# Optimization experiments

Hardware: AMD Instinct MI355X
Metric: run time of the kernel (lower is better)

Reference implementation:

```python
import jax, jax.numpy as jnp
import numpy as np

B, N, K = 4, 1500, 30
NODE_F, EDGE_F, H = 1024, 128, 128
L, NUM_RBF, NUM_POS, NHEADS = 4, 16, 16, 4
DH = H // NHEADS
LN_EPS = 1e-6


def setup_inputs() -> dict:
    key = jax.random.key(0)
    ks = jax.random.split(key, 16)
    g = lambda k, shp: jax.random.normal(k, shp, jnp.float32) / np.sqrt(shp[-2] if len(shp) > 1 else 1.0)
    return {
        'X': jax.random.normal(ks[0], (B, N, 3), jnp.float32) * 10.0,
        'V': jax.random.normal(ks[1], (B, N, NODE_F), jnp.float32),
        'mask': jnp.ones((B, N), jnp.float32),
        'W_v': g(ks[2], (NODE_F, H)), 'b_v': jnp.zeros((H,), jnp.float32),
        'W_e': g(ks[3], (EDGE_F, H)), 'b_e': jnp.zeros((H,), jnp.float32),
        'W_edge': g(ks[4], (NUM_POS + NUM_RBF, EDGE_F)),
        'ln_e_g': jnp.ones((EDGE_F,), jnp.float32), 'ln_e_b': jnp.zeros((EDGE_F,), jnp.float32),
        'Wq': g(ks[5], (L, H, H)), 'Wk': g(ks[6], (L, 2 * H, H)),
        'Wv_a': g(ks[7], (L, 2 * H, H)), 'Wo': g(ks[8], (L, H, H)),
        'ln1_g': jnp.ones((L, H), jnp.float32), 'ln1_b': jnp.zeros((L, H), jnp.float32),
        'ln2_g': jnp.ones((L, H), jnp.float32), 'ln2_b': jnp.zeros((L, H), jnp.float32),
        'W_ff1': g(ks[9], (L, H, 4 * H)), 'b_ff1': jnp.zeros((L, 4 * H), jnp.float32),
        'W_ff2': g(ks[10], (L, 4 * H, H)), 'b_ff2': jnp.zeros((L, H), jnp.float32),
        'W_out': g(ks[11], (H, 1)), 'b_out': jnp.zeros((1,), jnp.float32),
    }


def _layer_norm(x, gamma, beta):
    mu = jnp.mean(x, -1, keepdims=True)
    var = jnp.var(x, -1, keepdims=True)
    return gamma * (x - mu) / jnp.sqrt(var + LN_EPS) + beta


def _gather_nodes(nodes, idx):
    # nodes [B,N,C], idx [B,N,K] -> [B,N,K,C]
    return jax.vmap(lambda n, i: n[i])(nodes, idx)


def reference(X, V, mask, W_v, b_v, W_e, b_e, W_edge, ln_e_g, ln_e_b, Wq, Wk, Wv_a, Wo,
              ln1_g, ln1_b, ln2_g, ln2_b, W_ff1, b_ff1, W_ff2, b_ff2, W_out, b_out):
    # ---- EdgeFeatures: masked pairwise distances + kNN topk ----
    mask2 = mask[:, :, None] * mask[:, None, :]            # [B,N,N]
    dX = X[:, :, None, :] - X[:, None, :, :]               # [B,N,N,3]
    D = mask2 * jnp.sqrt(jnp.sum(dX * dX, -1) + 1e-6)
    D_adj = D + (1.0 - mask2) * jnp.max(D, -1, keepdims=True)
    negD, E_idx = jax.lax.top_k(-D_adj, K)                 # k smallest distances
    D_nb = -negD                                           # [B,N,K]
    # RBF of neighbor distances
    mu = jnp.linspace(0.0, 20.0, NUM_RBF)
    sigma = 20.0 / NUM_RBF
    rbf = jnp.exp(-(((D_nb[..., None] - mu) / sigma) ** 2))  # [B,N,K,NUM_RBF]
    # sinusoidal relative positional encodings of neighbor offsets
    ii = jnp.arange(N, dtype=jnp.float32)[None, :, None]
    d_rel = (E_idx.astype(jnp.float32) - ii)[..., None]
    freq = jnp.exp(jnp.arange(0, NUM_POS, 2, dtype=jnp.float32) * (-np.log(10000.0) / NUM_POS))
    ang = d_rel * freq
    pos = jnp.concatenate([jnp.cos(ang), jnp.sin(ang)], -1)  # [B,N,K,NUM_POS]
    E = jnp.concatenate([pos, rbf], -1) @ W_edge
    E = _layer_norm(E, ln_e_g, ln_e_b)                     # [B,N,K,EDGE_F]
    # ---- node / edge embeddings ----
    h_V = V @ W_v + b_v                                    # [B,N,H]
    h_E = E @ W_e + b_e                                    # [B,N,K,H]
    mask_attend = mask[:, :, None] * _gather_nodes(mask[..., None], E_idx)[..., 0]  # [B,N,K]
    neg_inf = jnp.float32(np.finfo(np.float32).min)
    # ---- encoder layers ----
    for l in range(L):
        h_EV = jnp.concatenate([h_E, _gather_nodes(h_V, E_idx)], -1)  # [B,N,K,2H]
        Q = (h_V @ Wq[l]).reshape(B, N, NHEADS, DH)
        Kh = (h_EV @ Wk[l]).reshape(B, N, K, NHEADS, DH)
        Vh = (h_EV @ Wv_a[l]).reshape(B, N, K, NHEADS, DH)
        logits = jnp.einsum('bnhd,bnkhd->bnhk', Q, Kh) / np.sqrt(DH)
        m = mask_attend[:, :, None, :]                     # [B,N,1,K]
        attend = jax.nn.softmax(jnp.where(m > 0, logits, neg_inf), -1) * m
        upd = jnp.einsum('bnhk,bnkhd->bnhd', attend, Vh).reshape(B, N, H) @ Wo[l]
        h_V = _layer_norm(h_V + upd, ln1_g[l], ln1_b[l])
        dh = jax.nn.relu(h_V @ W_ff1[l] + b_ff1[l]) @ W_ff2[l] + b_ff2[l]
        h_V = _layer_norm(h_V + dh, ln2_g[l], ln2_b[l])
        h_V = mask[..., None] * h_V
    return (h_V @ W_out + b_out)[..., 0]                   # [B,N] logits
```

## Files before the change

### kernel.cpp

```cpp
#include <hip/hip_runtime.h>
#include <hip/hip_bf16.h>
#include <math.h>

#define NB 4
#define NN 1500
#define KNB 30
#define H 128
#define NHEADS 4
#define FFH 512
#define NODE_FEAT 1024
#define NROWS (NB*NN)
#define LN_EPS 1e-6f

#define P_F32_STRIDE 384
#define P_BF16_STRIDE 768

#define WNT_STRIDE 67584

typedef __attribute__((ext_vector_type(8))) short s8v;
typedef __attribute__((ext_vector_type(4))) float f4v;

__device__ __forceinline__ float bf_lo(unsigned u){ union{unsigned i; float f;} v; v.i = u<<16; return v.f; }
__device__ __forceinline__ float bf_hi(unsigned u){ union{unsigned i; float f;} v; v.i = u & 0xffff0000u; return v.f; }

__device__ __forceinline__ void find_bucket30(
    const unsigned* hist, int base0, int t, int lane, int wave,
    int* wsum, int* res)
{
    int h[16], s = 0;
    const uint4* hp = (const uint4*)&hist[(t & 127) * 16];
    int sh = (t >> 7) << 4;
    uint4 w[4] = {hp[0], hp[1], hp[2], hp[3]};
#pragma unroll
    for (int i = 0; i < 4; i++) {
        h[i*4+0] = (w[i].x >> sh) & 0xffff;
        h[i*4+1] = (w[i].y >> sh) & 0xffff;
        h[i*4+2] = (w[i].z >> sh) & 0xffff;
        h[i*4+3] = (w[i].w >> sh) & 0xffff;
        s += h[i*4+0] + h[i*4+1] + h[i*4+2] + h[i*4+3];
    }
    int inc = s;
#pragma unroll
    for (int off = 1; off < 64; off <<= 1) {
        int o = __shfl_up(inc, off, 64);
        if (lane >= off) inc += o;
    }
    if (lane == 63) wsum[wave] = inc;
    __syncthreads();
    int base = base0 + inc - s;
    for (int w2 = 0; w2 < wave; w2++) base += wsum[w2];
    if (base < KNB && base + s >= KNB) {
        int running = base;
#pragma unroll
        for (int i = 0; i < 16; i++) {
            if (running < KNB && running + h[i] >= KNB) { res[0] = (t<<4)|i; res[1] = running; break; }
            running += h[i];
        }
    }
    __syncthreads();
}

__global__ __launch_bounds__(256) void topk_kernel(
    const float* __restrict__ X, const float* __restrict__ mask,
    int* __restrict__ E_idx, float* __restrict__ D_nb)
{
    int row = blockIdx.x;
    int b = row / NN;
    int t = threadIdx.x;
    int wave = t >> 6, lane = t & 63;
    __shared__ float d_adj[NN];
    __shared__ unsigned hist[2048];
    __shared__ float redw[4];
    __shared__ int   wsum[4];
    __shared__ int   res[2];
    __shared__ int   cand[64];
    __shared__ int   ncand;

    float xi0 = X[row*3+0], xi1 = X[row*3+1], xi2 = X[row*3+2];
    float mi = mask[row];

    float dr[6], m2r[6];
    float lmax = -1e30f;
#pragma unroll
    for (int q = 0; q < 6; q++) {
        int j = t + q*256;
        float d = 0.f, m2 = 0.f;
        if (j < NN) {
            float dx = xi0 - X[(b*NN+j)*3+0];
            float dy = xi1 - X[(b*NN+j)*3+1];
            float dz = xi2 - X[(b*NN+j)*3+2];
            d  = sqrtf(dx*dx + dy*dy + dz*dz + 1e-6f);
            m2 = mi * mask[b*NN+j];
            lmax = fmaxf(lmax, m2*d);
        }
        dr[q] = d; m2r[q] = m2;
    }
    for (int q = t; q < 2048; q += 256) hist[q] = 0;
#pragma unroll
    for (int off = 32; off > 0; off >>= 1)
        lmax = fmaxf(lmax, __shfl_xor(lmax, off, 64));
    if (lane == 0) redw[wave] = lmax;
    if (t == 0) ncand = 0;
    __syncthreads();
    float rowmax = fmaxf(fmaxf(redw[0], redw[1]), fmaxf(redw[2], redw[3]));

    unsigned kreg[6];
#pragma unroll
    for (int q = 0; q < 6; q++) {
        int j = t + q*256;
        if (j < NN) {
            float dv = m2r[q]*dr[q] + (1.0f - m2r[q])*rowmax;
            d_adj[j] = dv;
            unsigned key = __float_as_uint(dv);
            kreg[q] = key;
            unsigned bkt = key >> 20;
            atomicAdd(&hist[bkt & 2047], 1u << ((bkt >> 11) << 4));
        } else kreg[q] = 0xFFFFFFFFu;
    }
    __syncthreads();

    find_bucket30(hist, 0, t, lane, wave, wsum, res);
    int B1 = res[0], nb1 = res[1];

    for (int q = t; q < 2048; q += 256) hist[q] = 0;
    __syncthreads();
#pragma unroll
    for (int q = 0; q < 6; q++) {
        if ((kreg[q] >> 20) == (unsigned)B1) {
            unsigned bkt = (kreg[q] >> 8) & 0xFFF;
            atomicAdd(&hist[bkt & 2047], 1u << ((bkt >> 11) << 4));
        }
    }
    __syncthreads();

    find_bucket30(hist, nb1, t, lane, wave, wsum, res);
    unsigned Bfull = ((unsigned)B1 << 12) | (unsigned)res[0];

#pragma unroll
    for (int q = 0; q < 6; q++) {
        if ((kreg[q] >> 8) <= Bfull) {
            int slot = atomicAdd(&ncand, 1);
            if (slot < 64) cand[slot] = t + q*256;
        }
    }
    __syncthreads();

    if (wave == 0) {
        int nc = min(ncand, 64);
        if (lane < nc) {
            int j = cand[lane];
            float v = d_adj[j];
            int rank = 0;
            for (int m = 0; m < nc; m++) {
                int jm = cand[m];
                float vm = d_adj[jm];
                rank += (vm < v || (vm == v && jm < j)) ? 1 : 0;
            }
            if (rank < KNB) {
                E_idx[row*KNB + rank] = j;
                D_nb[row*KNB + rank]  = v;
            }
        }
    }
}

__global__ __launch_bounds__(256) void wprep_edge_kernel(
    const float* __restrict__ W_edge, __hip_bfloat16* __restrict__ W_edge_t)
{
    int tid = blockIdx.x*256 + threadIdx.x;
    int n = tid >> 5, k = tid & 31;
    W_edge_t[tid] = __float2bfloat16(W_edge[k*H + n]);
}

__global__ __launch_bounds__(256) void edge_kernel(
    const int* __restrict__ E_idx, const float* __restrict__ D_nb,
    const __hip_bfloat16* __restrict__ W_edge_t, const float* __restrict__ ln_g,
    const float* __restrict__ ln_b, __hip_bfloat16* __restrict__ E_ln,
    float* __restrict__ EMS)
{
    int g0 = blockIdx.x * 2;
    int t = threadIdx.x;
    int wave = t >> 6, lane = t & 63, lm = lane & 15, lq = lane >> 4;
    __shared__ __hip_bfloat16 Es[64*136];

    int row = wave*16 + lm;
    int rr = row < 60 ? row : 59;
    int node = g0 + (rr >= KNB ? 1 : 0);
    int e = node*KNB + (rr >= KNB ? rr - KNB : rr);
    float drel = (float)(E_idx[e] - (node % NN));
    float dnb  = D_nb[e];

    const float FR[8] = {1.f, 0.31622776601683794f, 0.1f, 0.031622776601683794f,
                         0.01f, 0.0031622776601683794f, 0.001f, 0.00031622776601683794f};
    union { s8v v; __hip_bfloat16 h[8]; } af;
    if (lq == 0) {
#pragma unroll
        for (int j = 0; j < 8; j++) af.h[j] = __float2bfloat16(cosf(drel*FR[j]));
    } else if (lq == 1) {
#pragma unroll
        for (int j = 0; j < 8; j++) af.h[j] = __float2bfloat16(sinf(drel*FR[j]));
    } else {
        int f0 = (lq-2)*8;
#pragma unroll
        for (int j = 0; j < 8; j++) {
            float mu = (20.0f/15.0f) * (float)(f0+j);
            float z = (dnb - mu) * 0.8f;
            af.h[j] = __float2bfloat16(expf(-z*z));
        }
    }

    f4v acc[8];
#pragma unroll
    for (int nt = 0; nt < 8; nt++) {
        s8v bf = *(const s8v*)&W_edge_t[(nt*16+lm)*32 + lq*8];
        f4v z = {0.f,0.f,0.f,0.f};
        acc[nt] = __builtin_amdgcn_mfma_f32_16x16x32_bf16(af.v, bf, z, 0,0,0);
    }

    float gv[8], bv[8];
#pragma unroll
    for (int nt = 0; nt < 8; nt++) { gv[nt] = ln_g[nt*16+lm]; bv[nt] = ln_b[nt*16+lm]; }
#pragma unroll
    for (int r = 0; r < 4; r++) {
        float sm = 0.f, sq = 0.f;
#pragma unroll
        for (int nt = 0; nt < 8; nt++) { float x = acc[nt][r]; sm += x; sq += x*x; }
#pragma unroll
        for (int m = 1; m < 16; m <<= 1) {
            sm += __shfl_xor(sm, m, 64);
            sq += __shfl_xor(sq, m, 64);
        }
        float mu = sm * (1.0f/H);
        float rs = rsqrtf(sq*(1.0f/H) - mu*mu + LN_EPS);
        int erow = wave*16 + lq*4 + r;
        if (lm == 0 && erow < 60) {
            EMS[(g0*KNB + erow)*2]     = rs;
            EMS[(g0*KNB + erow)*2 + 1] = mu*rs;
        }
#pragma unroll
        for (int nt = 0; nt < 8; nt++)
            Es[erow*136 + nt*16 + lm] =
                __float2bfloat16(gv[nt]*(acc[nt][r]-mu)*rs + bv[nt]);
    }
    __syncthreads();

    __hip_bfloat16* dst = E_ln + (size_t)g0*KNB*H;
    for (int q = t; q < 960; q += 256) {
        int r = q >> 4, c8 = (q & 15) * 8;
        *(s8v*)&dst[r*H + c8] = *(const s8v*)&Es[r*136 + c8];
    }
}

__global__ __launch_bounds__(256) void wprep_v_kernel(
    const float* __restrict__ W_v, __hip_bfloat16* __restrict__ Wv_t)
{
    int tid = blockIdx.x*256 + threadIdx.x;
    int n = tid & 127, k = tid >> 7;
    Wv_t[(size_t)n*NODE_FEAT + k] = __float2bfloat16(W_v[k*H + n]);
}

__global__ __launch_bounds__(128) void wprep_kv_kernel(
    const float* __restrict__ W_e, const float* __restrict__ b_e,
    const float* __restrict__ Wk, const float* __restrict__ Wv,
    float* __restrict__ Wkv_f, float* __restrict__ bias_kv)
{
    int l = blockIdx.x >> 8;
    int n = blockIdx.x & 255;
    int t = threadIdx.x;
    int col = n & 127;
    const float* W = (n < 128) ? (Wk + l*2*H*H) : (Wv + l*2*H*H);
    __shared__ float wcol[128];
    wcol[t] = W[t*H + col];
    __syncthreads();
    float a = 0.f;
    for (int c = 0; c < H; c += 4) {
        float4 we = *(const float4*)&W_e[t*H + c];
        a += we.x*wcol[c] + we.y*wcol[c+1] + we.z*wcol[c+2] + we.w*wcol[c+3];
    }
    Wkv_f[(size_t)(l*256 + n)*H + t] = a;
    if (t == 0) {
        float bsum = 0.f;
        for (int c = 0; c < H; c++) bsum += b_e[c]*wcol[c];
        bias_kv[l*256 + n] = bsum;
    }
}

__global__ __launch_bounds__(128) void wprep_m_kernel(
    const float* __restrict__ Wkv_f, const float* __restrict__ W_edge,
    const float* __restrict__ ln_e_g,
    float* __restrict__ M_buf, float* __restrict__ vg_buf)
{
    int l = blockIdx.x >> 7;
    int n = blockIdx.x & 127;
    int t = threadIdx.x;
    __shared__ float wg_s[128];
    wg_s[t] = Wkv_f[(size_t)(l*256 + n)*H + t] * ln_e_g[t];
    __syncthreads();
    if (t < 32) {
        float a = 0.f;
        for (int e = 0; e < 128; e++) a += wg_s[e] * W_edge[t*H + e];
        M_buf[((size_t)(l*128 + n))*32 + t] = a;
    } else if (t == 32) {
        float a = 0.f;
        for (int e = 0; e < 128; e++) a += wg_s[e];
        vg_buf[l*128 + n] = a;
    }
}

__global__ __launch_bounds__(128) void wprep_q2_kernel(
    const float* __restrict__ Wq, const float* __restrict__ M_buf,
    const float* __restrict__ vg_buf, __hip_bfloat16* __restrict__ Wn_t)
{
    int l = blockIdx.x >> 7;
    int c = blockIdx.x & 127;
    int t = threadIdx.x;
    int h = t >> 5, f = t & 31;
    __shared__ float wq_s[128];
    wq_s[t] = Wq[(size_t)l*16384 + c*128 + t];
    __syncthreads();
    float a = 0.f;
#pragma unroll
    for (int d = 0; d < 32; d++)
        a += wq_s[h*32 + d] * M_buf[((size_t)(l*128 + h*32 + d))*32 + f];
    Wn_t[(size_t)l*WNT_STRIDE + (128 + t)*H + c] = __float2bfloat16(a);
    if (t < 4) {
        float b = 0.f;
        for (int d = 0; d < 32; d++)
            b += wq_s[t*32 + d] * vg_buf[l*128 + t*32 + d];
        Wn_t[(size_t)l*WNT_STRIDE + (256 + t)*H + c] = __float2bfloat16(b);
    }
    if (t < 12) Wn_t[(size_t)l*WNT_STRIDE + (260 + t)*H + c] = __float2bfloat16(0.f);
}

__global__ __launch_bounds__(128) void wprep_op_kernel(
    const float* __restrict__ Wo, const float* __restrict__ Wkv_f,
    __hip_bfloat16* __restrict__ WoU_t)
{
    int l = blockIdx.x / 640;
    int kk = blockIdx.x - l*640;
    int n = threadIdx.x;
    __shared__ float wev[32];
    if (kk < 512) {
        int h = kk >> 7;
        int e = kk & 127;
        if (n < 32) wev[n] = Wkv_f[(size_t)(l*256 + 128 + h*32 + n)*H + e];
    }
    __syncthreads();
    float v;
    if (kk < 512) {
        int h = kk >> 7;
        float a = 0.f;
#pragma unroll
        for (int d = 0; d < 32; d++)
            a += wev[d]*Wo[(size_t)l*16384 + (h*32+d)*128 + n];
        v = a;
    } else {
        v = Wo[(size_t)l*16384 + (kk-512)*128 + n];
    }
    WoU_t[((size_t)l*128 + n)*640 + kk] = __float2bfloat16(v);
}

__global__ __launch_bounds__(256) void wprep_post_kernel(
    const float* __restrict__ Wf1, const float* __restrict__ Wf2,
    const float* __restrict__ Wq, const float* __restrict__ Wk,
    const float* __restrict__ Wv,
    __hip_bfloat16* __restrict__ Wf1_t, __hip_bfloat16* __restrict__ Wf2_t,
    __hip_bfloat16* __restrict__ Wn_t)
{
    int id = blockIdx.x*256 + threadIdx.x;
    int l = id / 180224;
    int r = id - l*180224;
    float v; __hip_bfloat16* dst;
    if (r < 65536) {
        int n = r >> 7, k = r & 127;
        v = Wf1[(size_t)l*65536 + k*512 + n];
        dst = Wf1_t + (size_t)l*65536 + r;
    } else if (r < 131072) {
        int rr = r - 65536;
        int n = rr >> 9, k = rr & 511;
        v = Wf2[(size_t)l*65536 + k*128 + n];
        dst = Wf2_t + (size_t)l*65536 + rr;
    } else if (r < 147456) {
        int rr = r - 131072;
        int n = rr >> 7, k = rr & 127;
        v = Wq[(size_t)l*16384 + k*128 + n];
        dst = Wn_t + (size_t)l*WNT_STRIDE + rr;
    } else {
        int rr = r - 147456;
        int n = rr >> 7, k = rr & 127;
        v = (n < 128) ? Wk[(size_t)l*32768 + (128+k)*128 + n]
                      : Wv[(size_t)l*32768 + (128+k)*128 + (n-128)];
        dst = Wn_t + (size_t)l*WNT_STRIDE + 272*H + rr;
    }
    *dst = __float2bfloat16(v);
}

__global__ __launch_bounds__(512) void hv_init_kernel(
    const float* __restrict__ V, const __hip_bfloat16* __restrict__ Wv_t,
    const float* __restrict__ b_v, float* __restrict__ hv,
    const __hip_bfloat16* __restrict__ Wn_t, float* __restrict__ P,
    __hip_bfloat16* __restrict__ PKV, float* __restrict__ qg_buf)
{
    int row0 = blockIdx.x * 32;
    int t = threadIdx.x;
    int wave = t >> 6, lane = t & 63, lm = lane & 15, lq = lane >> 4;
    __shared__ __hip_bfloat16 Vs[32*1032];
    __shared__ __hip_bfloat16 zs[32*136];

    for (int q = t; q < 8192; q += 512) {
        int r = q >> 8, c4 = (q & 255) * 4;
        int gr = row0 + r; if (gr > NROWS-1) gr = NROWS-1;
        float4 v4 = *(const float4*)&V[(size_t)gr*NODE_FEAT + c4];
        union { ushort u[4]; uint2 w; } pk;
        pk.u[0] = __bfloat16_as_ushort(__float2bfloat16(v4.x));
        pk.u[1] = __bfloat16_as_ushort(__float2bfloat16(v4.y));
        pk.u[2] = __bfloat16_as_ushort(__float2bfloat16(v4.z));
        pk.u[3] = __bfloat16_as_ushort(__float2bfloat16(v4.w));
        *(uint2*)&Vs[r*1032 + c4] = pk.w;
    }
    __syncthreads();

    {
        int cc = wave*16 + lm;
        float b = b_v[cc];
        f4v a0 = {0.f,0.f,0.f,0.f}, a1 = a0;
        for (int ks = 0; ks < 32; ks++) {
            s8v wf = *(const s8v*)&Wv_t[(size_t)(wave*16+lm)*NODE_FEAT + ks*32 + lq*8];
            s8v f0 = *(const s8v*)&Vs[lm*1032 + ks*32 + lq*8];
            s8v f1 = *(const s8v*)&Vs[(16+lm)*1032 + ks*32 + lq*8];
            a0 = __builtin_amdgcn_mfma_f32_16x16x32_bf16(f0, wf, a0, 0,0,0);
            a1 = __builtin_amdgcn_mfma_f32_16x16x32_bf16(f1, wf, a1, 0,0,0);
        }
#pragma unroll
        for (int r = 0; r < 4; r++) {
            int rr0 = lq*4 + r, rr1 = 16 + lq*4 + r;
            int g0 = row0 + rr0, g1 = row0 + rr1;
            float v0 = a0[r] + b, v1 = a1[r] + b;
            if (g0 < NROWS) hv[(size_t)g0*H + cc] = v0;
            if (g1 < NROWS) hv[(size_t)g1*H + cc] = v1;
            zs[rr0*136+cc] = __float2bfloat16(v0);
            zs[rr1*136+cc] = __float2bfloat16(v1);
        }
    }
    __syncthreads();

    __hip_bfloat16* Pb = (__hip_bfloat16*)P;
    for (int ntl = 0; ntl < 5; ntl++) {
        int nt = wave*5 + ntl;
        if (nt >= 33) break;
        int cc = nt*16 + lm;
        f4v a0 = {0.f,0.f,0.f,0.f}, a1 = a0;
#pragma unroll
        for (int ks = 0; ks < 4; ks++) {
            s8v wf = *(const s8v*)&Wn_t[(size_t)(nt*16+lm)*H + ks*32 + lq*8];
            s8v f0 = *(const s8v*)&zs[lm*136 + ks*32 + lq*8];
            s8v f1 = *(const s8v*)&zs[(16+lm)*136 + ks*32 + lq*8];
            a0 = __builtin_amdgcn_mfma_f32_16x16x32_bf16(f0, wf, a0, 0,0,0);
            a1 = __builtin_amdgcn_mfma_f32_16x16x32_bf16(f1, wf, a1, 0,0,0);
        }
#pragma unroll
        for (int mt = 0; mt < 2; mt++) {
            f4v* ap = mt ? &a1 : &a0;
#pragma unroll
            for (int r = 0; r < 4; r++) {
                int rr = row0 + mt*16 + lq*4 + r;
                if (rr < NROWS) {
                    float av = (*ap)[r];
                    if (cc < 128)
                        P[(size_t)rr*P_F32_STRIDE + cc] = av;
                    else if (cc < 256)
                        Pb[(size_t)rr*P_BF16_STRIDE + 640 + (cc-128)] = __float2bfloat16(av);
                    else if (cc < 272) {
                        if (cc < 260) qg_buf[rr*4 + (cc-256)] = av;
                    } else
                        PKV[(size_t)rr*256 + (cc-272)] = __float2bfloat16(av);
                }
            }
        }
    }
}

__global__ __launch_bounds__(256) void attn_kernel(
    const __hip_bfloat16* __restrict__ E_ln, const float* __restrict__ biasv,
    float* __restrict__ P, const __hip_bfloat16* __restrict__ PKV,
    const int* __restrict__ E_idx, const float* __restrict__ D_nb,
    const float* __restrict__ EMS, const float* __restrict__ qg_buf,
    const float* __restrict__ mask)
{
    int g0 = blockIdx.x * 2;
    int t = threadIdx.x;
    int wave = t >> 6, lane = t & 63, lm = lane & 15, lq = lane >> 4;
    __shared__ __hip_bfloat16 Es[60*136];
    __shared__ __hip_bfloat16 Ps[60*40];
    __shared__ __hip_bfloat16 Qps[2*136];
    __shared__ float Qs[2*128];
    __shared__ float att_s[2*128];
    __shared__ float ssum[8];
    __shared__ float mv_s[60];
    __shared__ float rs_s[60], murs_s[60];
    __shared__ float qgs[8];
    __shared__ int   nbr[60];

    const __hip_bfloat16* hebase = E_ln + (size_t)g0*KNB*H;
    for (int q = t; q < 960; q += 256) {
        int r = q >> 4, c8 = (q & 15) * 8;
        *(s8v*)&Es[r*136 + c8] = *(const s8v*)&hebase[r*H + c8];
    }
    const __hip_bfloat16* Pb = (const __hip_bfloat16*)P;
    if (t < 32) {
        int node = t >> 4, c8 = (t & 15)*8;
        *(s8v*)&Qps[node*136 + c8] = *(const s8v*)&Pb[(size_t)(g0+node)*P_BF16_STRIDE + 640 + c8];
    }
    {
        int node = t >> 7, c = t & 127;
        Qs[t] = P[(size_t)(g0+node)*P_F32_STRIDE + c];
    }
    if (t < 60) {
        int gn = g0 + t/30;
        int b = gn / NN;
        int idx = E_idx[gn*KNB + (t%30)];
        nbr[t]  = b*NN + idx;
        mv_s[t] = mask[gn] * mask[b*NN + idx];
        float2 em = ((const float2*)EMS)[g0*KNB + t];
        rs_s[t] = em.x; murs_s[t] = em.y;
    }
    if (t < 8) qgs[t] = qg_buf[(g0 + (t>>2))*4 + (t&3)];
    if (t < 240) {
        int r = t >> 2, seg = t & 3;
        int gn = g0 + r/30;
        int e = gn*KNB + (r%30);
        float drel = (float)(E_idx[e] - (gn % NN));
        float dnb  = D_nb[e];
        const float FR[8] = {1.f, 0.31622776601683794f, 0.1f, 0.031622776601683794f,
                             0.01f, 0.0031622776601683794f, 0.001f, 0.00031622776601683794f};
        union { s8v v; __hip_bfloat16 h[8]; } pf;
        if (seg == 0) {
#pragma unroll
            for (int j = 0; j < 8; j++) pf.h[j] = __float2bfloat16(__cosf(drel*FR[j]));
        } else if (seg == 1) {
#pragma unroll
            for (int j = 0; j < 8; j++) pf.h[j] = __float2bfloat16(__sinf(drel*FR[j]));
        } else {
            int f0 = (seg-2)*8;
#pragma unroll
            for (int j = 0; j < 8; j++) {
                float mu = (20.0f/15.0f) * (float)(f0+j);
                float z = (dnb - mu) * 0.8f;
                pf.h[j] = __float2bfloat16(__expf(-z*z));
            }
        }
        *(s8v*)&Ps[r*40 + seg*8] = pf.v;
    }
    __syncthreads();

    if (t < 240) {
        int node = t/120, tt = t%120, h = tt/30, kk = tt%30;
        int r = node*30 + kk;
        const uint4* pp = (const uint4*)&Ps[r*40];
        const uint4* qp = (const uint4*)&Qps[node*136 + h*32];
        float a = 0.f;
#pragma unroll
        for (int j = 0; j < 4; j++) {
            uint4 e4 = pp[j], q4 = qp[j];
            a += bf_lo(e4.x)*bf_lo(q4.x) + bf_hi(e4.x)*bf_hi(q4.x);
            a += bf_lo(e4.y)*bf_lo(q4.y) + bf_hi(e4.y)*bf_hi(q4.y);
            a += bf_lo(e4.z)*bf_lo(q4.z) + bf_hi(e4.z)*bf_hi(q4.z);
            a += bf_lo(e4.w)*bf_lo(q4.w) + bf_hi(e4.w)*bf_hi(q4.w);
        }
        a = rs_s[r]*a - murs_s[r]*qgs[node*4 + h];
        const uint4* kb = (const uint4*)(PKV + (size_t)nbr[r]*256 + h*32);
        const float* q = &Qs[node*128 + h*32];
#pragma unroll
        for (int j = 0; j < 4; j++) {
            uint4 u = kb[j];
            const float* q8 = q + j*8;
            a += q8[0]*bf_lo(u.x) + q8[1]*bf_hi(u.x)
               + q8[2]*bf_lo(u.y) + q8[3]*bf_hi(u.y)
               + q8[4]*bf_lo(u.z) + q8[5]*bf_hi(u.z)
               + q8[6]*bf_lo(u.w) + q8[7]*bf_hi(u.w);
        }
        att_s[node*128 + h*32 + kk] =
            (mv_s[r] > 0.f) ? a*0.17677669529663687f : -3.4028235e38f;
    }
    __syncthreads();

    if (wave < 2) {
        int node = wave, h = lq, j = lm;
        float* ap = &att_s[node*128 + h*32];
        const float* mp = &mv_s[node*30];
        float a0 = ap[j];
        float a1 = (j+16 < KNB) ? ap[j+16] : -3.4028235e38f;
        float mx = fmaxf(a0, a1);
#pragma unroll
        for (int m = 1; m < 16; m <<= 1) mx = fmaxf(mx, __shfl_xor(mx, m, 64));
        float e0 = __expf(a0 - mx);
        float e1 = (j+16 < KNB) ? __expf(a1 - mx) : 0.f;
        float s = e0 + e1;
#pragma unroll
        for (int m = 1; m < 16; m <<= 1) s += __shfl_xor(s, m, 64);
        float inv = 1.0f / s;
        float w0 = e0 * inv * mp[j];
        float w1 = (j+16 < KNB) ? e1 * inv * mp[j+16] : 0.f;
        ap[j] = w0;
        if (j+16 < KNB) ap[j+16] = w1;
        float ss = w0 + w1;
#pragma unroll
        for (int m = 1; m < 16; m <<= 1) ss += __shfl_xor(ss, m, 64);
        if (j == 0) ssum[node*4 + h] = ss;
    }
    __syncthreads();

    {
        int node = t >> 7, c = t & 127, h = c >> 5;
        __hip_bfloat16* Ub = (__hip_bfloat16*)P + (size_t)(g0+node)*P_BF16_STRIDE;
        const float* ap = &att_s[node*128];
        const int* nb = &nbr[node*30];

        float u = ssum[node*4 + h] * biasv[c];
        const float* ah = ap + h*32;
        for (int k = 0; k < KNB; k++)
            u += ah[k] * __bfloat162float(PKV[(size_t)nb[k]*256 + 128 + c]);
        Ub[512 + c] = __float2bfloat16(u);

        float s0 = 0.f, s1 = 0.f, s2 = 0.f, s3 = 0.f;
        for (int k = 0; k < KNB; k++) {
            float e = __bfloat162float(Es[(node*30+k)*136 + c]);
            s0 += ap[k]      * e;
            s1 += ap[32+k]   * e;
            s2 += ap[64+k]   * e;
            s3 += ap[96+k]   * e;
        }
        Ub[c]       = __float2bfloat16(s0);
        Ub[128 + c] = __float2bfloat16(s1);
        Ub[256 + c] = __float2bfloat16(s2);
        Ub[384 + c] = __float2bfloat16(s3);
    }
}

__global__ __launch_bounds__(512) void post_kernel(
    float* __restrict__ hv, float* __restrict__ P,
    __hip_bfloat16* __restrict__ PKV, float* __restrict__ qg_buf,
    const float* __restrict__ mask,
    const __hip_bfloat16* __restrict__ WoU_t,
    const float* __restrict__ ln1g, const float* __restrict__ ln1b,
    const float* __restrict__ ln2g, const float* __restrict__ ln2b,
    const __hip_bfloat16* __restrict__ Wf1_t, const float* __restrict__ bf1,
    const __hip_bfloat16* __restrict__ Wf2_t, const float* __restrict__ bf2,
    const __hip_bfloat16* __restrict__ Wn_t,
    const float* __restrict__ W_out, const float* __restrict__ b_out,
    float* __restrict__ out)
{
    int row0 = blockIdx.x * 32;
    int t = threadIdx.x;
    int wave = t >> 6, lane = t & 63, lm = lane & 15, lq = lane >> 4;

    __shared__ __hip_bfloat16 AusT1[32*648];
    __shared__ float xs[32*132];
    __shared__ __hip_bfloat16 yz[32*136];
    __hip_bfloat16* Aus = AusT1;
    __hip_bfloat16* t1  = AusT1;

    const __hip_bfloat16* Pbc = (const __hip_bfloat16*)P;
    for (int q = t; q < 2560; q += 512) {
        int r = q/80, c8 = (q%80)*8;
        int gr = row0 + r; if (gr > NROWS-1) gr = NROWS-1;
        *(s8v*)&Aus[r*648 + c8] = *(const s8v*)&Pbc[(size_t)gr*P_BF16_STRIDE + c8];
    }
    __syncthreads();

    {
        int cc = wave*16 + lm;
        f4v a0 = {0.f,0.f,0.f,0.f}, a1 = a0;
        for (int ks = 0; ks < 20; ks++) {
            s8v wf = *(const s8v*)&WoU_t[(size_t)(wave*16+lm)*640 + ks*32 + lq*8];
            s8v f0 = *(const s8v*)&Aus[lm*648 + ks*32 + lq*8];
            s8v f1 = *(const s8v*)&Aus[(16+lm)*648 + ks*32 + lq*8];
            a0 = __builtin_amdgcn_mfma_f32_16x16x32_bf16(f0, wf, a0, 0,0,0);
            a1 = __builtin_amdgcn_mfma_f32_16x16x32_bf16(f1, wf, a1, 0,0,0);
        }
#pragma unroll
        for (int r = 0; r < 4; r++) {
            int rr0 = lq*4 + r, rr1 = 16 + lq*4 + r;
            int g0 = row0 + rr0; if (g0 > NROWS-1) g0 = NROWS-1;
            int g1 = row0 + rr1; if (g1 > NROWS-1) g1 = NROWS-1;
            xs[rr0*132+cc] = hv[(size_t)g0*128 + cc] + a0[r];
            xs[rr1*132+cc] = hv[(size_t)g1*128 + cc] + a1[r];
        }
    }
    __syncthreads();

    {
        float g0 = ln1g[lane], g1 = ln1g[64+lane];
        float b0 = ln1b[lane], b1 = ln1b[64+lane];
#pragma unroll
        for (int i = 0; i < 4; i++) {
            int r = wave*4 + i;
            float x0 = xs[r*132 + lane], x1 = xs[r*132 + 64 + lane];
            float sm = x0 + x1, sq = x0*x0 + x1*x1;
#pragma unroll
            for (int m = 1; m < 64; m <<= 1) {
                sm += __shfl_xor(sm, m, 64);
                sq += __shfl_xor(sq, m, 64);
            }
            float mu = sm*(1.0f/H);
            float rs = rsqrtf(sq*(1.0f/H) - mu*mu + LN_EPS);
            float v0 = g0*(x0-mu)*rs + b0, v1 = g1*(x1-mu)*rs + b1;
            xs[r*132 + lane] = v0; xs[r*132 + 64 + lane] = v1;
            yz[r*136 + lane] = __float2bfloat16(v0);
            yz[r*136 + 64 + lane] = __float2bfloat16(v1);
        }
    }
    __syncthreads();

    for (int ntl = 0; ntl < 4; ntl++) {
        int nt = wave*4 + ntl;
        int cc = nt*16 + lm;
        float b = bf1[cc];
        f4v a0 = {0.f,0.f,0.f,0.f}, a1 = a0;
#pragma unroll
        for (int ks = 0; ks < 4; ks++) {
            s8v wf = *(const s8v*)&Wf1_t[(size_t)(nt*16+lm)*128 + ks*32 + lq*8];
            s8v f0 = *(const s8v*)&yz[lm*136 + ks*32 + lq*8];
            s8v f1 = *(const s8v*)&yz[(16+lm)*136 + ks*32 + lq*8];
            a0 = __builtin_amdgcn_mfma_f32_16x16x32_bf16(f0, wf, a0, 0,0,0);
            a1 = __builtin_amdgcn_mfma_f32_16x16x32_bf16(f1, wf, a1, 0,0,0);
        }
#pragma unroll
        for (int r = 0; r < 4; r++) {
            t1[(lq*4+r)*520 + cc]      = __float2bfloat16(fmaxf(a0[r]+b, 0.f));
            t1[(16+lq*4+r)*520 + cc]   = __float2bfloat16(fmaxf(a1[r]+b, 0.f));
        }
    }
    __syncthreads();

    {
        int cc = wave*16 + lm;
        float b = bf2[cc];
        f4v a0 = {0.f,0.f,0.f,0.f}, a1 = a0;
        for (int ks = 0; ks < 16; ks++) {
            s8v wf = *(const s8v*)&Wf2_t[(size_t)(wave*16+lm)*512 + ks*32 + lq*8];
            s8v f0 = *(const s8v*)&t1[lm*520 + ks*32 + lq*8];
            s8v f1 = *(const s8v*)&t1[(16+lm)*520 + ks*32 + lq*8];
            a0 = __builtin_amdgcn_mfma_f32_16x16x32_bf16(f0, wf, a0, 0,0,0);
            a1 = __builtin_amdgcn_mfma_f32_16x16x32_bf16(f1, wf, a1, 0,0,0);
        }
#pragma unroll
        for (int r = 0; r < 4; r++) {
            int rr0 = lq*4 + r, rr1 = 16 + lq*4 + r;
            xs[rr0*132+cc] = xs[rr0*132+cc] + a0[r] + b;
            xs[rr1*132+cc] = xs[rr1*132+cc] + a1[r] + b;
        }
    }
    __syncthreads();

    {
        float g0 = ln2g[lane], g1 = ln2g[64+lane];
        float b0 = ln2b[lane], b1 = ln2b[64+lane];
        float wo0 = 0.f, wo1 = 0.f, bo = 0.f;
        if (!Wn_t) { wo0 = W_out[lane]; wo1 = W_out[64+lane]; bo = b_out[0]; }
#pragma unroll
        for (int i = 0; i < 4; i++) {
            int r = wave*4 + i;
            int gr = row0 + r;
            float mk = mask[gr > NROWS-1 ? NROWS-1 : gr];
            float x0 = xs[r*132 + lane], x1 = xs[r*132 + 64 + lane];
            float sm = x0 + x1, sq = x0*x0 + x1*x1;
#pragma unroll
            for (int m = 1; m < 64; m <<= 1) {
                sm += __shfl_xor(sm, m, 64);
                sq += __shfl_xor(sq, m, 64);
            }
            float mu = sm*(1.0f/H);
            float rs = rsqrtf(sq*(1.0f/H) - mu*mu + LN_EPS);
            float v0 = mk*(g0*(x0-mu)*rs + b0), v1 = mk*(g1*(x1-mu)*rs + b1);
            yz[r*136 + lane] = __float2bfloat16(v0);
            yz[r*136 + 64 + lane] = __float2bfloat16(v1);
            if (gr < NROWS) {
                hv[(size_t)gr*128 + lane] = v0;
                hv[(size_t)gr*128 + 64 + lane] = v1;
            }
            if (!Wn_t) {
                float o = v0*wo0 + v1*wo1;
#pragma unroll
                for (int m = 1; m < 64; m <<= 1) o += __shfl_xor(o, m, 64);
                if (lane == 0 && gr < NROWS) out[gr] = o + bo;
            }
        }
    }
    __syncthreads();

    if (Wn_t) {
        __hip_bfloat16* Pbw = (__hip_bfloat16*)P;
        for (int ntl = 0; ntl < 5; ntl++) {
            int nt = wave*5 + ntl;
            if (nt >= 33) break;
            int cc = nt*16 + lm;
            f4v a0 = {0.f,0.f,0.f,0.f}, a1 = a0;
#pragma unroll
            for (int ks = 0; ks < 4; ks++) {
                s8v wf = *(const s8v*)&Wn_t[(size_t)(nt*16+lm)*128 + ks*32 + lq*8];
                s8v f0 = *(const s8v*)&yz[lm*136 + ks*32 + lq*8];
                s8v f1 = *(const s8v*)&yz[(16+lm)*136 + ks*32 + lq*8];
                a0 = __builtin_amdgcn_mfma_f32_16x16x32_bf16(f0, wf, a0, 0,0,0);
                a1 = __builtin_amdgcn_mfma_f32_16x16x32_bf16(f1, wf, a1, 0,0,0);
            }
#pragma unroll
            for (int mt = 0; mt < 2; mt++) {
                f4v* ap = mt ? &a1 : &a0;
#pragma unroll
                for (int r = 0; r < 4; r++) {
                    int rr = row0 + mt*16 + lq*4 + r;
                    if (rr < NROWS) {
                        float av = (*ap)[r];
                        if (cc < 128)
                            P[(size_t)rr*P_F32_STRIDE + cc] = av;
                        else if (cc < 256)
                            Pbw[(size_t)rr*P_BF16_STRIDE + 640 + (cc-128)] = __float2bfloat16(av);
                        else if (cc < 272) {
                            if (cc < 260) qg_buf[rr*4 + (cc-256)] = av;
                        } else
                            PKV[(size_t)rr*256 + (cc-272)] = __float2bfloat16(av);
                    }
                }
            }
        }
    }
}

extern "C" void kernel_launch(void* const* d_in, const int* in_sizes, int n_in,
                              void* d_out, int out_size, void* d_ws, size_t ws_size,
                              hipStream_t stream)
{
    const float* X      = (const float*)d_in[0];
    const float* V      = (const float*)d_in[1];
    const float* mask   = (const float*)d_in[2];
    const float* W_v    = (const float*)d_in[3];
    const float* b_v    = (const float*)d_in[4];
    const float* W_e    = (const float*)d_in[5];
    const float* b_e    = (const float*)d_in[6];
    const float* W_edge = (const float*)d_in[7];
    const float* ln_e_g = (const float*)d_in[8];
    const float* ln_e_b = (const float*)d_in[9];
    const float* Wq     = (const float*)d_in[10];
    const float* Wk     = (const float*)d_in[11];
    const float* Wv_a   = (const float*)d_in[12];
    const float* Wo     = (const float*)d_in[13];
    const float* ln1g   = (const float*)d_in[14];
    const float* ln1b   = (const float*)d_in[15];
    const float* ln2g   = (const float*)d_in[16];
    const float* ln2b   = (const float*)d_in[17];
    const float* Wf1    = (const float*)d_in[18];
    const float* bf1    = (const float*)d_in[19];
    const float* Wf2    = (const float*)d_in[20];
    const float* bf2    = (const float*)d_in[21];
    const float* W_out  = (const float*)d_in[22];
    const float* b_out  = (const float*)d_in[23];
    float* out = (float*)d_out;

    char* ws = (char*)d_ws;
    int*            E_idx    = (int*)ws;
    float*          D_nb     = (float*)(ws + 720000);
    __hip_bfloat16* E_ln     = (__hip_bfloat16*)(ws + 1440000);
    float*          hv       = (float*)(ws + 47520000);
    float*          bias_kv  = (float*)(ws + 50592000);
    float*          Wkv_f    = (float*)(ws + 50596096);
    __hip_bfloat16* Wn_t     = (__hip_bfloat16*)(ws + 51120384);
    __hip_bfloat16* WoU_t    = (__hip_bfloat16*)(ws + 52037888);
    __hip_bfloat16* Wf1_t    = (__hip_bfloat16*)(ws + 52693248);
    __hip_bfloat16* Wf2_t    = (__hip_bfloat16*)(ws + 53217536);
    __hip_bfloat16* Wv_t     = (__hip_bfloat16*)(ws + 53741824);
    __hip_bfloat16* W_edge_t = (__hip_bfloat16*)(ws + 54003968);
    __hip_bfloat16* PKV      = (__hip_bfloat16*)(ws + 54012160);
    float*          P        = (float*)(ws + 57084160);
    float*          EMS      = (float*)(ws + 66300160);
    float*          M_buf    = (float*)(ws + 67740160);
    float*          vg_buf   = (float*)(ws + 67805696);
    float*          qg_buf   = (float*)(ws + 67807744);

    topk_kernel<<<NROWS, 256, 0, stream>>>(X, mask, E_idx, D_nb);
    wprep_edge_kernel<<<16, 256, 0, stream>>>(W_edge, W_edge_t);
    edge_kernel<<<NROWS/2, 256, 0, stream>>>(E_idx, D_nb, W_edge_t, ln_e_g, ln_e_b, E_ln, EMS);
    wprep_kv_kernel<<<1024, 128, 0, stream>>>(W_e, b_e, Wk, Wv_a, Wkv_f, bias_kv);
    wprep_m_kernel<<<512, 128, 0, stream>>>(Wkv_f, W_edge, ln_e_g, M_buf, vg_buf);
    wprep_q2_kernel<<<512, 128, 0, stream>>>(Wq, M_buf, vg_buf, Wn_t);
    wprep_op_kernel<<<2560, 128, 0, stream>>>(Wo, Wkv_f, WoU_t);
    wprep_post_kernel<<<2816, 256, 0, stream>>>(Wf1, Wf2, Wq, Wk, Wv_a,
                                                Wf1_t, Wf2_t, Wn_t);
    wprep_v_kernel<<<512, 256, 0, stream>>>(W_v, Wv_t);
    hv_init_kernel<<<(NROWS+31)/32, 512, 0, stream>>>(V, Wv_t, b_v, hv, Wn_t, P, PKV, qg_buf);

    for (int l = 0; l < 4; l++) {
        attn_kernel<<<NROWS/2, 256, 0, stream>>>(
            E_ln, bias_kv + l*256 + 128, P, PKV, E_idx, D_nb, EMS, qg_buf, mask);
        post_kernel<<<(NROWS+31)/32, 512, 0, stream>>>(
            hv, P, PKV, qg_buf, mask, WoU_t + (size_t)l*81920,
            ln1g + l*H, ln1b + l*H, ln2g + l*H, ln2b + l*H,
            Wf1_t + (size_t)l*65536, bf1 + l*FFH,
            Wf2_t + (size_t)l*65536, bf2 + l*H,
            (l < 3) ? (Wn_t + (size_t)(l+1)*WNT_STRIDE) : (const __hip_bfloat16*)nullptr,
            W_out, b_out, out);
    }
}
```

Measured before the change: 417.8 us.

## Fold edge layernorm and edge projection into output weights, drop materialized E_ln

The layer-normalized edge features are no longer written to global memory. The attention kernel now aggregates the raw 32-wide edge inputs weighted by attention times the LN inverse std, plus per-head mean terms. The edge LN gain, bias and W_edge are folded into a precomputed combined output weight. This shrinks the post-kernel reduction dimension from 640 to 288 and removes a large E_ln write and its per-layer reads, at the cost of extra weight-prep kernels and bf16 rounding of the folded weights.

After: 397.6 us. 4.8% less time.

```diff
diff --git a/kernel.cpp b/kernel.cpp
--- a/kernel.cpp
+++ b/kernel.cpp
@@ -14,6 +14,7 @@
 
 #define P_F32_STRIDE 384
 #define P_BF16_STRIDE 768
+#define UK 288
 
 #define WNT_STRIDE 67584
 
@@ -174,14 +175,11 @@
 
 __global__ __launch_bounds__(256) void edge_kernel(
     const int* __restrict__ E_idx, const float* __restrict__ D_nb,
-    const __hip_bfloat16* __restrict__ W_edge_t, const float* __restrict__ ln_g,
-    const float* __restrict__ ln_b, __hip_bfloat16* __restrict__ E_ln,
-    float* __restrict__ EMS)
+    const __hip_bfloat16* __restrict__ W_edge_t, float* __restrict__ EMS)
 {
     int g0 = blockIdx.x * 2;
     int t = threadIdx.x;
     int wave = t >> 6, lane = t & 63, lm = lane & 15, lq = lane >> 4;
-    __shared__ __hip_bfloat16 Es[64*136];
 
     int row = wave*16 + lm;
     int rr = row < 60 ? row : 59;
@@ -217,9 +215,6 @@
         acc[nt] = __builtin_amdgcn_mfma_f32_16x16x32_bf16(af.v, bf, z, 0,0,0);
     }
 
-    float gv[8], bv[8];
-#pragma unroll
-    for (int nt = 0; nt < 8; nt++) { gv[nt] = ln_g[nt*16+lm]; bv[nt] = ln_b[nt*16+lm]; }
 #pragma unroll
     for (int r = 0; r < 4; r++) {
         float sm = 0.f, sq = 0.f;
@@ -237,17 +232,6 @@
             EMS[(g0*KNB + erow)*2]     = rs;
             EMS[(g0*KNB + erow)*2 + 1] = mu*rs;
         }
-#pragma unroll
-        for (int nt = 0; nt < 8; nt++)
-            Es[erow*136 + nt*16 + lm] =
-                __float2bfloat16(gv[nt]*(acc[nt][r]-mu)*rs + bv[nt]);
-    }
-    __syncthreads();
-
-    __hip_bfloat16* dst = E_ln + (size_t)g0*KNB*H;
-    for (int q = t; q < 960; q += 256) {
-        int r = q >> 4, c8 = (q & 15) * 8;
-        *(s8v*)&dst[r*H + c8] = *(const s8v*)&Es[r*136 + c8];
     }
 }
 
@@ -332,32 +316,44 @@
     if (t < 12) Wn_t[(size_t)l*WNT_STRIDE + (260 + t)*H + c] = __float2bfloat16(0.f);
 }
 
+__global__ __launch_bounds__(128) void wprep_op2_kernel(
+    const float* __restrict__ Wo, const float* __restrict__ Wkv_f,
+    const float* __restrict__ W_edge, const float* __restrict__ ln_e_g,
+    const float* __restrict__ ln_e_b, __hip_bfloat16* __restrict__ WoU_t)
+{
+    int l = blockIdx.x >> 9;
+    int hn = blockIdx.x & 511;
+    int h = hn >> 7, n = hn & 127;
+    int e = threadIdx.x;
+    __shared__ float tg[128], tb[128];
+    float tmp = 0.f;
+    const float* wo = Wo + (size_t)l*16384 + (h*32)*128 + n;
+    for (int d = 0; d < 32; d++)
+        tmp += Wkv_f[(size_t)(l*256 + 128 + h*32 + d)*H + e] * wo[d*128];
+    tg[e] = ln_e_g[e] * tmp;
+    tb[e] = ln_e_b[e] * tmp;
+    __syncthreads();
+    if (e < 32) {
+        float a = 0.f;
+        for (int ee = 0; ee < 128; ee++) a += W_edge[e*H + ee] * tg[ee];
+        WoU_t[((size_t)l*128 + n)*UK + h*32 + e] = __float2bfloat16(a);
+    } else if (e == 32) {
+        float a = 0.f, b = 0.f;
+        for (int ee = 0; ee < 128; ee++) { a += tg[ee]; b += tb[ee]; }
+        WoU_t[((size_t)l*128 + n)*UK + 128 + h] = __float2bfloat16(-a);
+        WoU_t[((size_t)l*128 + n)*UK + 132 + h] = __float2bfloat16(b);
+    }
+}
+
 __global__ __launch_bounds__(128) void wprep_op_kernel(
-    const float* __restrict__ Wo, const float* __restrict__ Wkv_f,
-    __hip_bfloat16* __restrict__ WoU_t)
-{
-    int l = blockIdx.x / 640;
-    int kk = blockIdx.x - l*640;
+    const float* __restrict__ Wo, __hip_bfloat16* __restrict__ WoU_t)
+{
+    int l = blockIdx.x / 152;
+    int kk = 136 + (blockIdx.x % 152);
     int n = threadIdx.x;
-    __shared__ float wev[32];
-    if (kk < 512) {
-        int h = kk >> 7;
-        int e = kk & 127;
-        if (n < 32) wev[n] = Wkv_f[(size_t)(l*256 + 128 + h*32 + n)*H + e];
-    }
-    __syncthreads();
-    float v;
-    if (kk < 512) {
-        int h = kk >> 7;
-        float a = 0.f;
-#pragma unroll
-        for (int d = 0; d < 32; d++)
-            a += wev[d]*Wo[(size_t)l*16384 + (h*32+d)*128 + n];
-        v = a;
-    } else {
-        v = Wo[(size_t)l*16384 + (kk-512)*128 + n];
-    }
-    WoU_t[((size_t)l*128 + n)*640 + kk] = __float2bfloat16(v);
+    float v = 0.f;
+    if (kk >= 144 && kk < 272) v = Wo[(size_t)l*16384 + (kk-144)*128 + n];
+    WoU_t[((size_t)l*128 + n)*UK + kk] = __float2bfloat16(v);
 }
 
 __global__ __launch_bounds__(256) void wprep_post_kernel(
@@ -481,7 +477,7 @@
 }
 
 __global__ __launch_bounds__(256) void attn_kernel(
-    const __hip_bfloat16* __restrict__ E_ln, const float* __restrict__ biasv,
+    const float* __restrict__ biasv,
     float* __restrict__ P, const __hip_bfloat16* __restrict__ PKV,
     const int* __restrict__ E_idx, const float* __restrict__ D_nb,
     const float* __restrict__ EMS, const float* __restrict__ qg_buf,
@@ -490,7 +486,6 @@
     int g0 = blockIdx.x * 2;
     int t = threadIdx.x;
     int wave = t >> 6, lane = t & 63, lm = lane & 15, lq = lane >> 4;
-    __shared__ __hip_bfloat16 Es[60*136];
     __shared__ __hip_bfloat16 Ps[60*40];
     __shared__ __hip_bfloat16 Qps[2*136];
     __shared__ float Qs[2*128];
@@ -501,11 +496,6 @@
     __shared__ float qgs[8];
     __shared__ int   nbr[60];
 
-    const __hip_bfloat16* hebase = E_ln + (size_t)g0*KNB*H;
-    for (int q = t; q < 960; q += 256) {
-        int r = q >> 4, c8 = (q & 15) * 8;
-        *(s8v*)&Es[r*136 + c8] = *(const s8v*)&hebase[r*H + c8];
-    }
     const __hip_bfloat16* Pb = (const __hip_bfloat16*)P;
     if (t < 32) {
         int node = t >> 4, c8 = (t & 15)*8;
@@ -611,29 +601,31 @@
     __syncthreads();
 
     {
-        int node = t >> 7, c = t & 127, h = c >> 5;
+        int node = t >> 7, c = t & 127, h = c >> 5, f = c & 31;
         __hip_bfloat16* Ub = (__hip_bfloat16*)P + (size_t)(g0+node)*P_BF16_STRIDE;
         const float* ap = &att_s[node*128];
         const int* nb = &nbr[node*30];
+        const float* ah = ap + h*32;
 
         float u = ssum[node*4 + h] * biasv[c];
-        const float* ah = ap + h*32;
         for (int k = 0; k < KNB; k++)
             u += ah[k] * __bfloat162float(PKV[(size_t)nb[k]*256 + 128 + c]);
-        Ub[512 + c] = __float2bfloat16(u);
-
-        float s0 = 0.f, s1 = 0.f, s2 = 0.f, s3 = 0.f;
-        for (int k = 0; k < KNB; k++) {
-            float e = __bfloat162float(Es[(node*30+k)*136 + c]);
-            s0 += ap[k]      * e;
-            s1 += ap[32+k]   * e;
-            s2 += ap[64+k]   * e;
-            s3 += ap[96+k]   * e;
-        }
-        Ub[c]       = __float2bfloat16(s0);
-        Ub[128 + c] = __float2bfloat16(s1);
-        Ub[256 + c] = __float2bfloat16(s2);
-        Ub[384 + c] = __float2bfloat16(s3);
+        Ub[144 + c] = __float2bfloat16(u);
+
+        float pb = 0.f;
+        for (int k = 0; k < KNB; k++)
+            pb += ah[k] * rs_s[node*30+k] * __bfloat162float(Ps[(node*30+k)*40 + f]);
+        Ub[c] = __float2bfloat16(pb);
+
+        if (c < 4) {
+            const float* ah2 = ap + c*32;
+            float sb = 0.f;
+            for (int k = 0; k < KNB; k++) sb += ah2[k] * murs_s[node*30+k];
+            Ub[128 + c] = __float2bfloat16(sb);
+            Ub[132 + c] = __float2bfloat16(ssum[node*4 + c]);
+        }
+        if (c < 8)  Ub[136 + c] = __float2bfloat16(0.f);
+        if (c >= 8 && c < 24) Ub[264 + c] = __float2bfloat16(0.f);
     }
 }
 
@@ -654,27 +646,27 @@
     int t = threadIdx.x;
     int wave = t >> 6, lane = t & 63, lm = lane & 15, lq = lane >> 4;
 
-    __shared__ __hip_bfloat16 AusT1[32*648];
+    __shared__ __hip_bfloat16 AusT1[32*520];
     __shared__ float xs[32*132];
     __shared__ __hip_bfloat16 yz[32*136];
     __hip_bfloat16* Aus = AusT1;
     __hip_bfloat16* t1  = AusT1;
 
     const __hip_bfloat16* Pbc = (const __hip_bfloat16*)P;
-    for (int q = t; q < 2560; q += 512) {
-        int r = q/80, c8 = (q%80)*8;
+    for (int q = t; q < 1152; q += 512) {
+        int r = q/36, c8 = (q%36)*8;
         int gr = row0 + r; if (gr > NROWS-1) gr = NROWS-1;
-        *(s8v*)&Aus[r*648 + c8] = *(const s8v*)&Pbc[(size_t)gr*P_BF16_STRIDE + c8];
+        *(s8v*)&Aus[r*296 + c8] = *(const s8v*)&Pbc[(size_t)gr*P_BF16_STRIDE + c8];
     }
     __syncthreads();
 
     {
         int cc = wave*16 + lm;
         f4v a0 = {0.f,0.f,0.f,0.f}, a1 = a0;
-        for (int ks = 0; ks < 20; ks++) {
-            s8v wf = *(const s8v*)&WoU_t[(size_t)(wave*16+lm)*640 + ks*32 + lq*8];
-            s8v f0 = *(const s8v*)&Aus[lm*648 + ks*32 + lq*8];
-            s8v f1 = *(const s8v*)&Aus[(16+lm)*648 + ks*32 + lq*8];
+        for (int ks = 0; ks < 9; ks++) {
+            s8v wf = *(const s8v*)&WoU_t[(size_t)(wave*16+lm)*UK + ks*32 + lq*8];
+            s8v f0 = *(const s8v*)&Aus[lm*296 + ks*32 + lq*8];
+            s8v f1 = *(const s8v*)&Aus[(16+lm)*296 + ks*32 + lq*8];
             a0 = __builtin_amdgcn_mfma_f32_16x16x32_bf16(f0, wf, a0, 0,0,0);
             a1 = __builtin_amdgcn_mfma_f32_16x16x32_bf16(f1, wf, a1, 0,0,0);
         }
@@ -860,7 +852,6 @@
     char* ws = (char*)d_ws;
     int*            E_idx    = (int*)ws;
     float*          D_nb     = (float*)(ws + 720000);
-    __hip_bfloat16* E_ln     = (__hip_bfloat16*)(ws + 1440000);
     float*          hv       = (float*)(ws + 47520000);
     float*          bias_kv  = (float*)(ws + 50592000);
     float*          Wkv_f    = (float*)(ws + 50596096);
@@ -879,11 +870,12 @@
 
     topk_kernel<<<NROWS, 256, 0, stream>>>(X, mask, E_idx, D_nb);
     wprep_edge_kernel<<<16, 256, 0, stream>>>(W_edge, W_edge_t);
-    edge_kernel<<<NROWS/2, 256, 0, stream>>>(E_idx, D_nb, W_edge_t, ln_e_g, ln_e_b, E_ln, EMS);
+    edge_kernel<<<NROWS/2, 256, 0, stream>>>(E_idx, D_nb, W_edge_t, EMS);
     wprep_kv_kernel<<<1024, 128, 0, stream>>>(W_e, b_e, Wk, Wv_a, Wkv_f, bias_kv);
     wprep_m_kernel<<<512, 128, 0, stream>>>(Wkv_f, W_edge, ln_e_g, M_buf, vg_buf);
     wprep_q2_kernel<<<512, 128, 0, stream>>>(Wq, M_buf, vg_buf, Wn_t);
-    wprep_op_kernel<<<2560, 128, 0, stream>>>(Wo, Wkv_f, WoU_t);
+    wprep_op2_kernel<<<2048, 128, 0, stream>>>(Wo, Wkv_f, W_edge, ln_e_g, ln_e_b, WoU_t);
+    wprep_op_kernel<<<608, 128, 0, stream>>>(Wo, WoU_t);
     wprep_post_kernel<<<2816, 256, 0, stream>>>(Wf1, Wf2, Wq, Wk, Wv_a,
                                                 Wf1_t, Wf2_t, Wn_t);
     wprep_v_kernel<<<512, 256, 0, stream>>>(W_v, Wv_t);
@@ -891,9 +883,9 @@
 
     for (int l = 0; l < 4; l++) {
         attn_kernel<<<NROWS/2, 256, 0, stream>>>(
-            E_ln, bias_kv + l*256 + 128, P, PKV, E_idx, D_nb, EMS, qg_buf, mask);
+            bias_kv + l*256 + 128, P, PKV, E_idx, D_nb, EMS, qg_buf, mask);
         post_kernel<<<(NROWS+31)/32, 512, 0, stream>>>(
-            hv, P, PKV, qg_buf, mask, WoU_t + (size_t)l*81920,
+            hv, P, PKV, qg_buf, mask, WoU_t + (size_t)l*128*UK,
             ln1g + l*H, ln1b + l*H, ln2g + l*H, ln2b + l*H,
             Wf1_t + (size_t)l*65536, bf1 + l*FFH,
             Wf2_t + (size_t)l*65536, bf2 + l*H,
```
